# Optimization experiments

Hardware: AMD Instinct MI355X
Metric: run time of the kernel (lower is better)

The kernel has to match this reference:

```python
import jax, jax.numpy as jnp
import numpy as np
from jax import lax

EPS = 1e-5
DN = ('NCHW', 'OIHW', 'NCHW')


def setup_inputs() -> dict:
    key = jax.random.key(0)
    ks = jax.random.split(key, 26)
    f = lambda k, shape: jax.random.normal(k, shape, dtype=jnp.float32) * 0.05
    u = lambda k, shape: jax.random.uniform(k, shape, jnp.float32, 0.5, 1.5)
    B = 512
    return {
        'x': jax.random.normal(ks[0], (B, 3, 32, 32), jnp.float32),
        'conv1_w': f(ks[1], (64, 3, 3, 3)), 'conv1_b': f(ks[2], (64,)),
        'bn1_g': 1.0 + f(ks[3], (64,)), 'bn1_b': f(ks[4], (64,)),
        'bn1_m': f(ks[5], (64,)), 'bn1_v': u(ks[6], (64,)),
        'conv2_w': f(ks[7], (256, 64, 3, 3)), 'conv2_b': f(ks[8], (256,)),
        'bna_g': 1.0 + f(ks[9], (64, 4)), 'bna_b': f(ks[10], (64, 4)),
        'bna_m': f(ks[11], (64, 4)), 'bna_v': u(ks[12], (64, 4)),
        'tconv_w': f(ks[13], (64, 8, 4, 3, 3)), 'tconv_b': f(ks[14], (64, 8)),
        'bnb_g': 1.0 + f(ks[15], (64, 8)), 'bnb_b': f(ks[16], (64, 8)),
        'bnb_m': f(ks[17], (64, 8)), 'bnb_v': u(ks[18], (64, 8)),
        'lin_w': f(ks[19], (64, 9, 1152)), 'lin_b': f(ks[20], (64, 9)),
        'fc1_w': f(ks[21], (512, 576)), 'fc1_b': f(ks[22], (512,)),
        'fc2_w': f(ks[23], (100, 512)), 'fc2_b': f(ks[24], (100,)),
    }


def reference(x, conv1_w, conv1_b, bn1_g, bn1_b, bn1_m, bn1_v,
              conv2_w, conv2_b,
              bna_g, bna_b, bna_m, bna_v, tconv_w, tconv_b,
              bnb_g, bnb_b, bnb_m, bnb_v, lin_w, lin_b,
              fc1_w, fc1_b, fc2_w, fc2_b):
    B = x.shape[0]
    # features: Conv(3->64,k3) -> ReLU -> BN(64) -> Conv(64->256,k3) -> ReLU -> MaxPool2
    h = lax.conv_general_dilated(x, conv1_w, (1, 1), 'VALID', dimension_numbers=DN)
    h = jax.nn.relu(h + conv1_b[None, :, None, None])  # [B,64,30,30]
    h = (h - bn1_m[None, :, None, None]) * lax.rsqrt(bn1_v + EPS)[None, :, None, None] \
        * bn1_g[None, :, None, None] + bn1_b[None, :, None, None]
    h = lax.conv_general_dilated(h, conv2_w, (1, 1), 'VALID', dimension_numbers=DN)
    h = jax.nn.relu(h + conv2_b[None, :, None, None])  # [B,256,28,28]
    h = lax.reduce_window(h, -jnp.inf, lax.max, (1, 1, 2, 2), (1, 1, 2, 2), 'VALID')  # [B,256,14,14]

    # 64 towers: BN2d(4) -> Conv(4->8,k3) -> BN2d(8) -> Flatten -> Linear(1152->9)
    f4 = h.reshape(B, 64, 4, 14, 14)
    f4 = (f4 - bna_m[None, :, :, None, None]) * lax.rsqrt(bna_v + EPS)[None, :, :, None, None] \
        * bna_g[None, :, :, None, None] + bna_b[None, :, :, None, None]
    # grouped conv fuses all 64 towers: out channels 64*8=512, 4 in-channels per group
    t = lax.conv_general_dilated(f4.reshape(B, 256, 14, 14), tconv_w.reshape(512, 4, 3, 3),
                                 (1, 1), 'VALID', dimension_numbers=DN, feature_group_count=64)
    t = t + tconv_b.reshape(512)[None, :, None, None]  # [B,512,12,12]
    t = t.reshape(B, 64, 8, 12, 12)
    t = (t - bnb_m[None, :, :, None, None]) * lax.rsqrt(bnb_v + EPS)[None, :, :, None, None] \
        * bnb_g[None, :, :, None, None] + bnb_b[None, :, :, None, None]
    flat = t.reshape(B, 64, 8 * 12 * 12)
    tow = jnp.einsum('btf,tof->bto', flat, lin_w) + lin_b[None]  # [B,64,9]
    z = tow.reshape(B, 576)

    # classifier (dropout = identity in eval)
    h1 = jax.nn.relu(z @ fc1_w.T + fc1_b)
    return h1 @ fc2_w.T + fc2_b
```

## Files before the change

kernel.cpp:

```cpp
#include <hip/hip_runtime.h>
#include <hip/hip_bf16.h>

#define EPS 1e-5f

typedef __attribute__((ext_vector_type(8))) short bf16x8;
typedef __attribute__((ext_vector_type(4))) float f32x4;

__device__ __forceinline__ float b2f(unsigned short u) {
  union { unsigned int i; float f; } v; v.i = ((unsigned int)u) << 16; return v.f;
}
__device__ __forceinline__ unsigned short f2bu(float f) {
  __hip_bfloat16 h = __float2bfloat16(f);
  return *reinterpret_cast<unsigned short*>(&h);
}

__device__ __forceinline__ void g2l16(const void* g, void* l) {
  __builtin_amdgcn_global_load_lds(
      (__attribute__((address_space(1))) void*)((unsigned long long)g),
      (__attribute__((address_space(3))) void*)((unsigned long long)l), 16, 0, 0);
}

__global__ __launch_bounds__(256) void k_prep(
    const float* __restrict__ x, const float* __restrict__ w1,
    const float* __restrict__ cb, const float* __restrict__ bg,
    const float* __restrict__ bb, const float* __restrict__ bm,
    const float* __restrict__ bv, __hip_bfloat16* __restrict__ h1,
    const float* __restrict__ w2, __hip_bfloat16* __restrict__ w2s,
    const float* __restrict__ fw1, unsigned int* __restrict__ w1p,
    const float* __restrict__ fw2, unsigned int* __restrict__ w2p,
    const float* __restrict__ lw, const float* __restrict__ lb,
    const float* __restrict__ tw, const float* __restrict__ tb,
    const float* __restrict__ bag, const float* __restrict__ bab,
    const float* __restrict__ bam, const float* __restrict__ bav,
    const float* __restrict__ bbg, const float* __restrict__ bbb,
    const float* __restrict__ bbm, const float* __restrict__ bbv,
    float* __restrict__ Weff, float* __restrict__ beff) {
  __shared__ __align__(16) char smem[43008];
  int tid = threadIdx.x;
  int bi = blockIdx.x;

  if (bi < 64) {
    int t = bi;
    float* lws = (float*)smem;
    float* tws = (float*)(smem + 41472);
    float* part = (float*)(smem + 42624);
    {
      const float4* src = (const float4*)(lw + (size_t)t * 9 * 1152);
      float4* dst = (float4*)lws;
      for (int i = tid; i < 2592; i += 256) dst[i] = src[i];
    }
    for (int i = tid; i < 288; i += 256) {
      int o8 = i / 36, c = (i % 36) / 9, kk = i % 9;
      float sa = bag[t * 4 + c] * rsqrtf(bav[t * 4 + c] + EPS);
      float sb = bbg[t * 8 + o8] * rsqrtf(bbv[t * 8 + o8] + EPS);
      tws[i] = tw[((t * 8 + o8) * 4 + c) * 9 + kk] * sa * sb;
    }
    __syncthreads();
    if (tid < 252) {
      int j = tid / 28;
      int rem = tid % 28;
      int c = rem / 7, q = rem % 7;
      float acc[2][14];
#pragma unroll
      for (int pr = 0; pr < 2; pr++)
#pragma unroll
        for (int ix = 0; ix < 14; ix++) acc[pr][ix] = 0.f;
#pragma unroll 1
      for (int o8 = 0; o8 < 8; o8++) {
        float twr[9];
#pragma unroll
        for (int kk = 0; kk < 9; kk++) twr[kk] = tws[o8 * 36 + c * 9 + kk];
        float lwc[4][16];
#pragma unroll
        for (int cr = 0; cr < 4; cr++) {
          int y = 2 * q - 2 + cr;
          bool vld = (y >= 0) & (y <= 11);
          int ya = vld ? y : 0;
          const float* bp = lws + j * 1152 + o8 * 144 + ya * 12;
          float4 A = *(const float4*)bp;
          float4 B = *(const float4*)(bp + 4);
          float4 C = *(const float4*)(bp + 8);
          lwc[cr][0] = 0.f; lwc[cr][1] = 0.f; lwc[cr][14] = 0.f; lwc[cr][15] = 0.f;
          lwc[cr][2] = vld ? A.x : 0.f;  lwc[cr][3] = vld ? A.y : 0.f;
          lwc[cr][4] = vld ? A.z : 0.f;  lwc[cr][5] = vld ? A.w : 0.f;
          lwc[cr][6] = vld ? B.x : 0.f;  lwc[cr][7] = vld ? B.y : 0.f;
          lwc[cr][8] = vld ? B.z : 0.f;  lwc[cr][9] = vld ? B.w : 0.f;
          lwc[cr][10] = vld ? C.x : 0.f; lwc[cr][11] = vld ? C.y : 0.f;
          lwc[cr][12] = vld ? C.z : 0.f; lwc[cr][13] = vld ? C.w : 0.f;
        }
#pragma unroll
        for (int ky = 0; ky < 3; ky++)
#pragma unroll
          for (int kx = 0; kx < 3; kx++) {
            float wv = twr[ky * 3 + kx];
#pragma unroll
            for (int pr = 0; pr < 2; pr++)
#pragma unroll
              for (int ix = 0; ix < 14; ix++)
                acc[pr][ix] += lwc[pr - ky + 2][ix - kx + 2] * wv;
          }
      }
#pragma unroll
      for (int pr = 0; pr < 2; pr++)
#pragma unroll
        for (int ix = 0; ix < 14; ix++)
          Weff[(((size_t)(t * 9 + j)) * 196 + (2 * q + pr) * 14 + ix) * 4 + c] = acc[pr][ix];
    }
    if (tid < 72) {
      int j = tid / 8, o8 = tid % 8;
      float s = 0.f;
      const float* bp = lws + j * 1152 + o8 * 144;
      for (int i = 0; i < 144; i++) s += bp[i];
      float sb = bbg[t * 8 + o8] * rsqrtf(bbv[t * 8 + o8] + EPS);
      float bfov = sb * tb[t * 8 + o8] + bbb[t * 8 + o8] - bbm[t * 8 + o8] * sb;
      for (int c2 = 0; c2 < 4; c2++) {
        float sa2 = bag[t * 4 + c2] * rsqrtf(bav[t * 4 + c2] + EPS);
        float ha = bab[t * 4 + c2] - bam[t * 4 + c2] * sa2;
        float wsum = 0.f;
        for (int k = 0; k < 9; k++) wsum += tw[((t * 8 + o8) * 4 + c2) * 9 + k];
        bfov += sb * wsum * ha;
      }
      part[tid] = bfov * s;
    }
    __syncthreads();
    if (tid < 9) {
      float acc = lb[t * 9 + tid];
      for (int o8 = 0; o8 < 8; o8++) acc += part[tid * 8 + o8];
      beff[t * 9 + tid] = acc;
    }
  } else if (bi < 576) {
    int b = bi - 64;
    float* xs = (float*)smem;
    float* wsm = (float*)(smem + 13824);
    {
      const float4* src = (const float4*)(x + (size_t)b * 3072);
      for (int i = tid; i < 768; i += 256) {
        int ic = i >> 8, r = (i >> 3) & 31, v = i & 7;
        *(float4*)(xs + (ic * 32 + r) * 36 + v * 4) = src[i];
      }
      const float4* wsrc = (const float4*)w1;
      float4* wdst = (float4*)wsm;
      for (int i = tid; i < 432; i += 256) wdst[i] = wsrc[i];
    }
    __syncthreads();
    int oc = tid & 63;
    int xg = tid >> 6;
    float wr[27];
#pragma unroll
    for (int q = 0; q < 27; q++) wr[q] = wsm[oc * 27 + q];
    float bias = cb[oc];
    float sc = bg[oc] * rsqrtf(bv[oc] + EPS);
    float sh = bb[oc] - bm[oc] * sc;
    float rx[3][3][12];
#pragma unroll
    for (int ic = 0; ic < 3; ic++)
#pragma unroll
      for (int s = 0; s < 2; s++) {
        const float* rp = xs + (ic * 32 + s) * 36 + xg * 8;
        float4 A = *(const float4*)rp, B = *(const float4*)(rp + 4), C = *(const float4*)(rp + 8);
        rx[ic][s][0] = A.x; rx[ic][s][1] = A.y; rx[ic][s][2] = A.z; rx[ic][s][3] = A.w;
        rx[ic][s][4] = B.x; rx[ic][s][5] = B.y; rx[ic][s][6] = B.z; rx[ic][s][7] = B.w;
        rx[ic][s][8] = C.x; rx[ic][s][9] = C.y; rx[ic][s][10] = C.z; rx[ic][s][11] = C.w;
      }
    int nst = (xg == 3) ? 6 : 8;
    __hip_bfloat16* dst0 = h1 + (((size_t)b * 30) * 30 + xg * 8) * 64 + oc;
#pragma unroll 1
    for (int y3 = 0; y3 < 10; y3++) {
#pragma unroll
      for (int s = 0; s < 3; s++) {
        int y = y3 * 3 + s;
        int ls = (s + 2) % 3;
#pragma unroll
        for (int ic = 0; ic < 3; ic++) {
          const float* rp = xs + (ic * 32 + (y + 2)) * 36 + xg * 8;
          float4 A = *(const float4*)rp, B = *(const float4*)(rp + 4), C = *(const float4*)(rp + 8);
          rx[ic][ls][0] = A.x; rx[ic][ls][1] = A.y; rx[ic][ls][2] = A.z; rx[ic][ls][3] = A.w;
          rx[ic][ls][4] = B.x; rx[ic][ls][5] = B.y; rx[ic][ls][6] = B.z; rx[ic][ls][7] = B.w;
          rx[ic][ls][8] = C.x; rx[ic][ls][9] = C.y; rx[ic][ls][10] = C.z; rx[ic][ls][11] = C.w;
        }
        float o[8];
#pragma unroll
        for (int j = 0; j < 8; j++) o[j] = bias;
#pragma unroll
        for (int ic = 0; ic < 3; ic++)
#pragma unroll
          for (int ky = 0; ky < 3; ky++) {
            int sl = (s + ky) % 3;
#pragma unroll
            for (int kx = 0; kx < 3; kx++) {
              float wv = wr[ic * 9 + ky * 3 + kx];
#pragma unroll
              for (int j = 0; j < 8; j++) o[j] += rx[ic][sl][j + kx] * wv;
            }
          }
        __hip_bfloat16* dst = dst0 + (size_t)y * 30 * 64;
#pragma unroll
        for (int j = 0; j < 8; j++)
          if (j < nst) dst[(size_t)j * 64] = __float2bfloat16(fmaxf(o[j], 0.f) * sc + sh);
      }
    }
  } else if (bi < 1152) {
    int g = (bi - 576) * 256 + tid;
    int kk = g >> 14;
    int rem = g & 16383;
    int oc = rem >> 6, e = rem & 63;
    int es = e ^ ((oc & 7) << 3);
    w2s[(kk * 256 + oc) * 64 + es] = __float2bfloat16(w2[(oc * 64 + e) * 9 + kk]);
  } else {
    int g = (bi - 1152) * 256 + tid;
    {
      int kp = g >> 9, o = g & 511;
      unsigned int lo = f2bu(fw1[o * 576 + 2 * kp]);
      unsigned int hi = f2bu(fw1[o * 576 + 2 * kp + 1]);
      w1p[g] = lo | (hi << 16);
    }
    if (g < 25600) {
      int kp = g / 100, o = g % 100;
      unsigned int lo = f2bu(fw2[o * 512 + 2 * kp]);
      unsigned int hi = f2bu(fw2[o * 512 + 2 * kp + 1]);
      w2p[g] = lo | (hi << 16);
    }
  }
}

__global__ __launch_bounds__(512) void k2_conv2(
    const __hip_bfloat16* __restrict__ h1, const __hip_bfloat16* __restrict__ w2s,
    const float* __restrict__ c2b, const float* __restrict__ Weff,
    float* __restrict__ z) {
  __shared__ __align__(16) char lds[81920];
  int tid = threadIdx.x;
  int bid = blockIdx.x;
  int swz = (bid & 7) * 896 + (bid >> 3);
  int b = swz / 14, yp = swz % 14;
  int l = tid & 63, w = tid >> 6;

  int r = tid >> 3;
  int rc = r < 56 ? r : 55;
  int yl = rc >= 28 ? 1 : 0;
  int xx = rc - yl * 28;
  int ael = ((tid & 7) << 3) ^ ((rc & 7) << 3);
  const __hip_bfloat16* aSrc0 =
      h1 + (((size_t)(b * 30 + yp * 2 + yl)) * 30 + xx) * 64 + ael;
  const char* bSrc0 = (const char*)w2s;

  f32x4 acc[4][2];
#pragma unroll
  for (int m = 0; m < 4; m++)
#pragma unroll
    for (int n = 0; n < 2; n++) acc[m][n] = (f32x4){0.f, 0.f, 0.f, 0.f};

#define STAGE(kk, s)                                                            \
  {                                                                             \
    g2l16(aSrc0 + (((kk) / 3) * 30 + ((kk) % 3)) * 64,                          \
          lds + (s)*8192 + tid * 16);                                           \
    const char* bs = bSrc0 + (kk)*32768;                                        \
    _Pragma("unroll") for (int q = 0; q < 4; q++)                               \
        g2l16(bs + q * 8192 + tid * 16,                                         \
              lds + 16384 + (s)*32768 + q * 8192 + tid * 16);                   \
  }

  STAGE(0, 0);
#pragma unroll
  for (int c = 0; c < 9; c++) {
    __syncthreads();
    if (c < 8) STAGE(c + 1, (c + 1) & 1);
    char* aB = lds + (c & 1) * 8192;
    char* bB = lds + 16384 + (c & 1) * 32768;
#pragma unroll
    for (int ks = 0; ks < 2; ks++) {
      bf16x8 af[4], bfr[2];
      int kb = (ks * 32 + ((l >> 4) * 8)) * 2;
#pragma unroll
      for (int m = 0; m < 4; m++) {
        int row = m * 16 + (l & 15);
        af[m] = *(const bf16x8*)(aB + row * 128 + (kb ^ ((row & 7) << 4)));
      }
#pragma unroll
      for (int n = 0; n < 2; n++) {
        int oc = w * 32 + n * 16 + (l & 15);
        bfr[n] = *(const bf16x8*)(bB + oc * 128 + (kb ^ ((oc & 7) << 4)));
      }
#pragma unroll
      for (int m = 0; m < 4; m++)
#pragma unroll
        for (int n = 0; n < 2; n++)
          acc[m][n] = __builtin_amdgcn_mfma_f32_16x16x32_bf16(af[m], bfr[n], acc[m][n], 0, 0, 0);
    }
  }
#undef STAGE
  __syncthreads();

  unsigned short* ep = (unsigned short*)lds + w * 2304;
#pragma unroll
  for (int n = 0; n < 2; n++) {
    int col = n * 16 + (l & 15);
    float bias = c2b[w * 32 + col];
#pragma unroll
    for (int m = 0; m < 4; m++)
#pragma unroll
      for (int i = 0; i < 4; i++) {
        int row = m * 16 + ((l >> 4) * 4) + i;
        ep[row * 36 + col] = f2bu(fmaxf(acc[m][n][i] + bias, 0.f));
      }
  }
  __syncthreads();
  unsigned short* pool = (unsigned short*)(lds + 36864);
#pragma unroll
  for (int q = 0; q < 7; q++) {
    int xp = (l >> 5) * 7 + q;
    int col = l & 31;
    int base0 = (2 * xp) * 36 + col;
    float m0 = fmaxf(fmaxf(b2f(ep[base0]), b2f(ep[base0 + 36])),
                     fmaxf(b2f(ep[base0 + 28 * 36]), b2f(ep[base0 + 29 * 36])));
    pool[(w * 32 + col) * 14 + xp] = f2bu(m0);
  }
  __syncthreads();
#pragma unroll
  for (int rep = 0; rep < 2; rep++) {
    int tj = rep * 512 + tid;
    if (rep == 1 && tid >= 64) break;
    int t = tj / 9;
    const float4* wrow = (const float4*)(Weff + (size_t)tj * 784 + yp * 56);
    const unsigned short* pr = pool + t * 4 * 14;
    float s = 0.f;
#pragma unroll
    for (int xp = 0; xp < 14; xp++) {
      float4 wv = wrow[xp];
      s += wv.x * b2f(pr[xp]) + wv.y * b2f(pr[14 + xp]) +
           wv.z * b2f(pr[28 + xp]) + wv.w * b2f(pr[42 + xp]);
    }
    atomicAdd(z + (size_t)b * 576 + tj, s);
  }
}

__global__ __launch_bounds__(256) void k4_fc(
    const float* __restrict__ z, const float* __restrict__ beff,
    const unsigned int* __restrict__ w1p, const float* __restrict__ b1,
    const unsigned int* __restrict__ w2p, const float* __restrict__ b2,
    float* __restrict__ out) {
  __shared__ float zl[576];
  __shared__ float hl[512];
  int tid = threadIdx.x, b = blockIdx.x;
  for (int i = tid; i < 576; i += 256) zl[i] = z[(size_t)b * 576 + i] + beff[i];
  __syncthreads();
#pragma unroll
  for (int oo = 0; oo < 2; oo++) {
    int o = tid + oo * 256;
    float acc = b1[o];
#pragma unroll 4
    for (int kp = 0; kp < 288; kp++) {
      unsigned int u = w1p[kp * 512 + o];
      float2 zz = *(const float2*)(zl + 2 * kp);
      acc += zz.x * b2f((unsigned short)(u & 0xffff)) + zz.y * b2f((unsigned short)(u >> 16));
    }
    hl[o] = fmaxf(acc, 0.f);
  }
  __syncthreads();
  if (tid < 100) {
    float acc = b2[tid];
#pragma unroll 4
    for (int kp = 0; kp < 256; kp++) {
      unsigned int u = w2p[kp * 100 + tid];
      float2 hh = *(const float2*)(hl + 2 * kp);
      acc += hh.x * b2f((unsigned short)(u & 0xffff)) + hh.y * b2f((unsigned short)(u >> 16));
    }
    out[(size_t)b * 100 + tid] = acc;
  }
}

extern "C" void kernel_launch(void* const* d_in, const int* in_sizes, int n_in,
                              void* d_out, int out_size, void* d_ws, size_t ws_size,
                              hipStream_t stream) {
  const float* x    = (const float*)d_in[0];
  const float* w1   = (const float*)d_in[1];
  const float* c1b  = (const float*)d_in[2];
  const float* bn1g = (const float*)d_in[3];
  const float* bn1b = (const float*)d_in[4];
  const float* bn1m = (const float*)d_in[5];
  const float* bn1v = (const float*)d_in[6];
  const float* w2   = (const float*)d_in[7];
  const float* c2b  = (const float*)d_in[8];
  const float* bnag = (const float*)d_in[9];
  const float* bnab = (const float*)d_in[10];
  const float* bnam = (const float*)d_in[11];
  const float* bnav = (const float*)d_in[12];
  const float* tw   = (const float*)d_in[13];
  const float* tb   = (const float*)d_in[14];
  const float* bnbg = (const float*)d_in[15];
  const float* bnbb = (const float*)d_in[16];
  const float* bnbm = (const float*)d_in[17];
  const float* bnbv = (const float*)d_in[18];
  const float* linw = (const float*)d_in[19];
  const float* linb = (const float*)d_in[20];
  const float* fc1w = (const float*)d_in[21];
  const float* fc1b = (const float*)d_in[22];
  const float* fc2w = (const float*)d_in[23];
  const float* fc2b = (const float*)d_in[24];
  float* out = (float*)d_out;

  char* ws = (char*)d_ws;
  size_t off = 0;
  auto alloc = [&](size_t bytes) {
    char* q = ws + off;
    off += (bytes + 255) & ~(size_t)255;
    return q;
  };
  __hip_bfloat16* h1  = (__hip_bfloat16*)alloc(512ull * 30 * 30 * 64 * 2);
  __hip_bfloat16* w2s = (__hip_bfloat16*)alloc(9ull * 256 * 64 * 2);
  float* Weff = (float*)alloc(451584ull * 4);
  float* beff = (float*)alloc(576ull * 4);
  unsigned int* w1p = (unsigned int*)alloc(288ull * 512 * 4);
  unsigned int* w2p = (unsigned int*)alloc(256ull * 100 * 4);
  float* z    = (float*)alloc(512ull * 576 * 4);

  hipMemsetAsync(z, 0, 512ull * 576 * 4, stream);
  k_prep<<<1728, 256, 0, stream>>>(x, w1, c1b, bn1g, bn1b, bn1m, bn1v, h1,
                                   w2, w2s, fc1w, w1p, fc2w, w2p,
                                   linw, linb, tw, tb,
                                   bnag, bnab, bnam, bnav,
                                   bnbg, bnbb, bnbm, bnbv, Weff, beff);
  k2_conv2<<<512 * 14, 512, 0, stream>>>(h1, w2s, c2b, Weff, z);
  k4_fc<<<512, 256, 0, stream>>>(z, beff, w1p, fc1b, w2p, fc2b, out);
}
```

Baseline: 428.9 us.

## Transpose Weff layout for coalesced loads and prefetch weights before pooling

Reorders the Weff tensor so the 576 tower-output index is innermost, letting adjacent threads read consecutive float2 values instead of strided float4 rows. Half of each thread's weights are prefetched into registers before the epilogue and pooling stages so the global-load latency overlaps that work. The cost is extra register pressure from the 14 float2 prefetch buffer, and the producer kernel's writes to Weff become scattered.

Result: faster. 398.3 us (-7.1%).

```diff
diff --git a/kernel.cpp b/kernel.cpp
--- a/kernel.cpp
+++ b/kernel.cpp
@@ -104,7 +104,8 @@
       for (int pr = 0; pr < 2; pr++)
 #pragma unroll
         for (int ix = 0; ix < 14; ix++)
-          Weff[(((size_t)(t * 9 + j)) * 196 + (2 * q + pr) * 14 + ix) * 4 + c] = acc[pr][ix];
+          Weff[(((size_t)(2 * q + pr) * 28 + ix * 2 + (c >> 1)) * 576 + t * 9 + j) * 2 + (c & 1)] =
+              acc[pr][ix];
     }
     if (tid < 72) {
       int j = tid / 8, o8 = tid % 8;
@@ -290,6 +291,11 @@
 #undef STAGE
   __syncthreads();
 
+  const float2* wbase = (const float2*)Weff + (size_t)yp * 16128 + tid;
+  float2 wva[14];
+#pragma unroll
+  for (int k = 0; k < 14; k++) wva[k] = wbase[k * 576];
+
   unsigned short* ep = (unsigned short*)lds + w * 2304;
 #pragma unroll
   for (int n = 0; n < 2; n++) {
@@ -315,19 +321,34 @@
     pool[(w * 32 + col) * 14 + xp] = f2bu(m0);
   }
   __syncthreads();
-#pragma unroll
-  for (int rep = 0; rep < 2; rep++) {
-    int tj = rep * 512 + tid;
-    if (rep == 1 && tid >= 64) break;
+  {
+    int t = tid / 9;
+    const unsigned short* pr = pool + t * 56;
+    float s = 0.f;
+#pragma unroll
+    for (int k = 0; k < 14; k++) {
+      int ix = k >> 1, c2 = (k & 1) * 2;
+      s += wva[k].x * b2f(pr[c2 * 14 + ix]) + wva[k].y * b2f(pr[(c2 + 1) * 14 + ix]);
+    }
+#pragma unroll
+    for (int k = 14; k < 28; k++) {
+      int ix = k >> 1, c2 = (k & 1) * 2;
+      float2 wvk = wbase[k * 576];
+      s += wvk.x * b2f(pr[c2 * 14 + ix]) + wvk.y * b2f(pr[(c2 + 1) * 14 + ix]);
+    }
+    atomicAdd(z + (size_t)b * 576 + tid, s);
+  }
+  if (tid < 64) {
+    int tj = 512 + tid;
     int t = tj / 9;
-    const float4* wrow = (const float4*)(Weff + (size_t)tj * 784 + yp * 56);
-    const unsigned short* pr = pool + t * 4 * 14;
+    const float2* wb2 = (const float2*)Weff + (size_t)yp * 16128 + tj;
+    const unsigned short* pr = pool + t * 56;
     float s = 0.f;
 #pragma unroll
-    for (int xp = 0; xp < 14; xp++) {
-      float4 wv = wrow[xp];
-      s += wv.x * b2f(pr[xp]) + wv.y * b2f(pr[14 + xp]) +
-           wv.z * b2f(pr[28 + xp]) + wv.w * b2f(pr[42 + xp]);
+    for (int k = 0; k < 28; k++) {
+      int ix = k >> 1, c2 = (k & 1) * 2;
+      float2 wvk = wb2[k * 576];
+      s += wvk.x * b2f(pr[c2 * 14 + ix]) + wvk.y * b2f(pr[(c2 + 1) * 14 + ix]);
     }
     atomicAdd(z + (size_t)b * 576 + tj, s);
   }
```
